# Kernel tuning notes

Measured on AMD Instinct MI355X. Metric: run time of the kernel, lower is better.

Reference implementation:

```python
import jax, jax.numpy as jnp
import numpy as np

B, S = 32, 4096
QRYDIM, CTXDIM, ENCDIM = 512, 512, 256


def setup_inputs() -> dict:
    key = jax.random.key(0)
    ks = jax.random.split(key, 8)
    qry = jax.random.normal(ks[0], (B, QRYDIM), dtype=jnp.float32)
    ctx = jax.random.normal(ks[1], (B, S, CTXDIM), dtype=jnp.float32)
    ctx_mask = jax.random.randint(ks[2], (B, S), 0, 2, dtype=jnp.int32)
    # first Linear(qrydim+ctxdim, encdim): split into ctx-part and qry-part
    # (equivalent to concat([ctx, qry]) @ W1^T since concat order is [ctx, qry])
    sc1 = 1.0 / np.sqrt(QRYDIM + CTXDIM)
    Wc = jax.random.uniform(ks[3], (CTXDIM, ENCDIM), jnp.float32, -sc1, sc1)
    Wq = jax.random.uniform(ks[4], (QRYDIM, ENCDIM), jnp.float32, -sc1, sc1)
    b1 = jax.random.uniform(ks[5], (ENCDIM,), jnp.float32, -sc1, sc1)
    sc2 = 1.0 / np.sqrt(ENCDIM)
    w2 = jax.random.uniform(ks[6], (ENCDIM,), jnp.float32, -sc2, sc2)
    b2 = jax.random.uniform(ks[7], (), jnp.float32, -sc2, sc2)
    return {"qry": qry, "ctx": ctx, "ctx_mask": ctx_mask,
            "Wc": Wc, "Wq": Wq, "b1": b1, "w2": w2, "b2": b2}


def reference(qry, ctx, ctx_mask, Wc, Wq, b1, w2, b2):
    # hidden = tanh(concat([ctx, qry_broadcast]) @ W1 + b1), computed without
    # materializing the (B, S, CTXDIM+QRYDIM) concat tensor
    h_ctx = jnp.einsum('bsc,ce->bse', ctx, Wc)          # (B, S, E)
    h_qry = jnp.einsum('bq,qe->be', qry, Wq)            # (B, E)
    h = jnp.tanh(h_ctx + h_qry[:, None, :] + b1)        # (B, S, E)
    scores = jnp.einsum('bse,e->bs', h, w2) + b2        # (B, S)
    # additive log-mask, then softmax over seqlen
    scores = scores + jnp.log(ctx_mask.astype(jnp.float32))
    alphas = jax.nn.softmax(scores, axis=-1)            # (B, S)
    # weighted sum over context (values default to ctx)
    summary = jnp.einsum('bs,bsd->bd', alphas, ctx)     # (B, CTXDIM)
    return alphas, summary, scores
```

## Files before the change

### kernel.cpp

```cpp
#include <hip/hip_runtime.h>
#include <math.h>

#define BB 32
#define SS 4096
#define CD 512
#define ED 256

#define ALPHAS_OFF 0
#define SUMMARY_OFF (BB * SS)
#define SCORES_OFF (BB * SS + BB * CD)

#define NEG_BIG (-1.0e30f)

typedef __attribute__((ext_vector_type(8))) short short8;
typedef __attribute__((ext_vector_type(8))) unsigned short us8;
typedef __attribute__((ext_vector_type(4))) float f32x4;

__device__ __forceinline__ unsigned short f2bf(float f) {
    unsigned u = __float_as_uint(f);
    u += 0x7FFFu + ((u >> 16) & 1u);
    return (unsigned short)(u >> 16);
}
__device__ __forceinline__ float bf2f(unsigned short h) {
    return __uint_as_float(((unsigned)h) << 16);
}
__device__ __forceinline__ float fast_tanh(float x) {
    const float ex = __expf(2.0f * x);
    return 1.0f - __fdividef(2.0f, ex + 1.0f);
}

#define GLOAD_LDS16(g, l) __builtin_amdgcn_global_load_lds( \
    (const __attribute__((address_space(1))) void*)(g),     \
    (__attribute__((address_space(3))) void*)(l), 16, 0, 0)

#define WS_BH_OFF 32768
#define BPLANE 131072

__global__ void k_prep(const float* __restrict__ Wc, unsigned short* __restrict__ Bh,
                       unsigned short* __restrict__ Bl) {
    const int bid = blockIdx.x;
    const int l = threadIdx.x;
    const int e = (bid & 15) * 16 + (l & 15);
    const int kbase = (bid >> 4) * 32 + (l >> 4) * 8;
    const size_t off = ((size_t)bid * 64 + l) * 8;
#pragma unroll
    for (int j = 0; j < 8; ++j) {
        const float f = Wc[(size_t)(kbase + j) * ED + e];
        const unsigned short h = f2bf(f);
        Bh[off + j] = h;
        Bl[off + j] = f2bf(f - bf2f(h));
    }
}

__global__ void k_hq(const float* __restrict__ qry, const float* __restrict__ Wq,
                     const float* __restrict__ b1, float* __restrict__ hq,
                     float* __restrict__ out) {
    const int b = blockIdx.x;
    const int e = threadIdx.x;
    {
        float* scz = out + SCORES_OFF + b * SS;
#pragma unroll
        for (int i = 0; i < 16; ++i) scz[i * 256 + e] = 0.0f;
    }
    __shared__ float qs[CD];
    qs[e] = qry[b * CD + e];
    qs[e + 256] = qry[b * CD + e + 256];
    __syncthreads();
    float acc = b1[e];
#pragma unroll 8
    for (int c = 0; c < CD; ++c) {
        acc = fmaf(qs[c], Wq[c * ED + e], acc);
    }
    hq[b * ED + e] = acc;
}

#define ST 128
__global__ __launch_bounds__(512, 4)
void k_scores(const float* __restrict__ ctx,
              const unsigned short* __restrict__ Bh, const unsigned short* __restrict__ Bl,
              const float* __restrict__ hq, const float* __restrict__ w2,
              float* __restrict__ out) {
    const int b = blockIdx.y;
    const int stile = blockIdx.x >> 1;
    const int ehalf = blockIdx.x & 1;
    const int s0 = stile * ST;
    const int tid = threadIdx.x;
    const int w = tid >> 6;
    const int l = tid & 63;
    const int eq = w & 1;
    const int mq = w >> 1;

    __shared__ unsigned short BsH[2][8 * 64 * 8];
    __shared__ unsigned short BsL[2][8 * 64 * 8];
    __shared__ float red[2][ST];

    f32x4 acc[2][4];
#pragma unroll
    for (int mi = 0; mi < 2; ++mi)
#pragma unroll
        for (int t = 0; t < 4; ++t) acc[mi][t] = (f32x4)(0.0f);

    const float* ctx_b = ctx + (size_t)(b * SS + s0) * CD;

    const float* aptr0 = ctx_b + (size_t)(mq * 32 + (l & 15)) * CD + (l >> 4) * 8;
    const float* aptr1 = aptr0 + 16 * CD;

    const char* gBplane = (const char*)((w < 4) ? Bh : Bl);
    char* lBbase = (char*)((w < 4) ? &BsH[0][0] : &BsL[0][0]);
    const int wv = w & 3;
    const int bq = wv * 2048 + l * 16;
    const size_t gchunk0 = (size_t)(ehalf * 8) * 1024;

    float4 ra0[2], ra1[2];
    {
        const char* gsrc = gBplane + gchunk0 + bq;
        GLOAD_LDS16(gsrc, lBbase + bq);
        GLOAD_LDS16(gsrc + 1024, lBbase + bq + 1024);
    }
    __builtin_amdgcn_sched_barrier(0);
    ra0[0] = *(const float4*)(aptr0);
    ra1[0] = *(const float4*)(aptr0 + 4);
    ra0[1] = *(const float4*)(aptr1);
    ra1[1] = *(const float4*)(aptr1 + 4);
    __builtin_amdgcn_sched_barrier(0);
    asm volatile("s_waitcnt vmcnt(4)" ::: "memory");
    __builtin_amdgcn_sched_barrier(0);
    __builtin_amdgcn_s_barrier();
    __builtin_amdgcn_sched_barrier(0);

    int cur = 0;
    for (int c = 0; c < 16; ++c) {
        short8 ah[2], alo[2];
#pragma unroll
        for (int mi = 0; mi < 2; ++mi) {
            const float f[8] = {ra0[mi].x, ra0[mi].y, ra0[mi].z, ra0[mi].w,
                                ra1[mi].x, ra1[mi].y, ra1[mi].z, ra1[mi].w};
            short8 H, L;
#pragma unroll
            for (int j = 0; j < 8; ++j) {
                const unsigned short h = f2bf(f[j]);
                H[j] = (short)h;
                L[j] = (short)f2bf(f[j] - bf2f(h));
            }
            ah[mi] = H;
            alo[mi] = L;
        }
        __builtin_amdgcn_sched_barrier(0);

        if (c < 15) {
            const char* gsrc = gBplane + (size_t)(c + 1) * 16384 + gchunk0 + bq;
            char* ldst = lBbase + (cur ^ 1) * 8192 + bq;
            GLOAD_LDS16(gsrc, ldst);
            GLOAD_LDS16(gsrc + 1024, ldst + 1024);
        }
        __builtin_amdgcn_sched_barrier(0);
        if (c < 15) {
            ra0[0] = *(const float4*)(aptr0 + (c + 1) * 32);
            ra1[0] = *(const float4*)(aptr0 + (c + 1) * 32 + 4);
            ra0[1] = *(const float4*)(aptr1 + (c + 1) * 32);
            ra1[1] = *(const float4*)(aptr1 + (c + 1) * 32 + 4);
        }
        __builtin_amdgcn_sched_barrier(0);

        __builtin_amdgcn_s_setprio(1);
#pragma unroll
        for (int t = 0; t < 4; ++t) {
            const int le = eq * 4 + t;
            const int boff = (le * 64 + l) * 8;
            const short8 bh = *(const short8*)(&BsH[cur][boff]);
            const short8 bl = *(const short8*)(&BsL[cur][boff]);
#pragma unroll
            for (int mi = 0; mi < 2; ++mi) {
                acc[mi][t] = __builtin_amdgcn_mfma_f32_16x16x32_bf16(ah[mi], bh, acc[mi][t], 0, 0, 0);
                acc[mi][t] = __builtin_amdgcn_mfma_f32_16x16x32_bf16(alo[mi], bh, acc[mi][t], 0, 0, 0);
                acc[mi][t] = __builtin_amdgcn_mfma_f32_16x16x32_bf16(ah[mi], bl, acc[mi][t], 0, 0, 0);
            }
        }
        __builtin_amdgcn_s_setprio(0);

        __builtin_amdgcn_sched_barrier(0);
        asm volatile("s_waitcnt vmcnt(4)" ::: "memory");
        __builtin_amdgcn_sched_barrier(0);
        __builtin_amdgcn_s_barrier();
        __builtin_amdgcn_sched_barrier(0);
        cur ^= 1;
    }

    float hqr[4], w2r[4];
#pragma unroll
    for (int t = 0; t < 4; ++t) {
        const int e = (ehalf * 8 + eq * 4 + t) * 16 + (l & 15);
        hqr[t] = hq[b * ED + e];
        w2r[t] = w2[e];
    }

#pragma unroll
    for (int mi = 0; mi < 2; ++mi) {
#pragma unroll
        for (int reg = 0; reg < 4; ++reg) {
            float v = 0.0f;
#pragma unroll
            for (int t = 0; t < 4; ++t) {
                v += w2r[t] * fast_tanh(acc[mi][t][reg] + hqr[t]);
            }
            v += __shfl_xor(v, 1, 64);
            v += __shfl_xor(v, 2, 64);
            v += __shfl_xor(v, 4, 64);
            v += __shfl_xor(v, 8, 64);
            if ((l & 15) == 0) {
                const int row = (l >> 4) * 4 + reg;
                red[eq][(mq * 2 + mi) * 16 + row] = v;
            }
        }
    }
    __syncthreads();
    if (tid < ST) {
        atomicAdd(out + SCORES_OFF + b * SS + s0 + tid, red[0][tid] + red[1][tid]);
    }
}

__global__ void k_softmax(float* __restrict__ out, const int* __restrict__ mask,
                          const float* __restrict__ b2p) {
    const int b = blockIdx.x;
    const int tid = threadIdx.x;
    float* sc = out + SCORES_OFF + b * SS;
    float* al = out + ALPHAS_OFF + b * SS;

    {
        float* sm = out + SUMMARY_OFF + b * CD;
        sm[tid] = 0.0f;
        sm[tid + 256] = 0.0f;
    }

    const float b2v = b2p[0];

    __shared__ float red[4];
    __shared__ float bcast;
    const int lane = tid & 63;
    const int wave = tid >> 6;

    float loc[16];
    float mx = -INFINITY;
#pragma unroll
    for (int i = 0; i < 16; ++i) {
        const int s = i * 256 + tid;
        float v = sc[s] + b2v;
        if (mask[b * SS + s] == 0) v = NEG_BIG;
        sc[s] = v;
        loc[i] = v;
        mx = fmaxf(mx, v);
    }
    for (int off = 32; off >= 1; off >>= 1) mx = fmaxf(mx, __shfl_down(mx, off, 64));
    if (lane == 0) red[wave] = mx;
    __syncthreads();
    if (tid == 0) bcast = fmaxf(fmaxf(red[0], red[1]), fmaxf(red[2], red[3]));
    __syncthreads();
    const float mxall = bcast;

    float sum = 0.0f;
#pragma unroll
    for (int i = 0; i < 16; ++i) {
        const float ev = __expf(loc[i] - mxall);
        loc[i] = ev;
        sum += ev;
    }
    for (int off = 32; off >= 1; off >>= 1) sum += __shfl_down(sum, off, 64);
    if (lane == 0) red[wave] = sum;
    __syncthreads();
    if (tid == 0) bcast = red[0] + red[1] + red[2] + red[3];
    __syncthreads();
    const float inv = 1.0f / bcast;

#pragma unroll
    for (int i = 0; i < 16; ++i) al[i * 256 + tid] = loc[i] * inv;
}

#define SROWS 128
__global__ void k_summary(const float* __restrict__ ctx, const float* __restrict__ out_alphas,
                          float* __restrict__ out) {
    const int b = blockIdx.y;
    const int s0 = blockIdx.x * SROWS;
    const int t = threadIdx.x;
    const int sg = t >> 7;
    const int d = (t & 127) * 4;

    __shared__ float al[SROWS];
    if (t < SROWS) al[t] = out_alphas[ALPHAS_OFF + b * SS + s0 + t];
    __syncthreads();

    const float* base = ctx + (size_t)(b * SS + s0 + sg * 64) * CD + d;
    const float* alp = &al[sg * 64];
    float4 a0 = make_float4(0.f, 0.f, 0.f, 0.f);
    float4 a1 = a0, a2 = a0, a3 = a0;
#pragma unroll 2
    for (int i = 0; i < 16; ++i) {
        const int s = i * 4;
        const float w0 = alp[s + 0], w1 = alp[s + 1], w2_ = alp[s + 2], w3 = alp[s + 3];
        if (w0 != 0.0f) {
            const float4 v0 = *(const float4*)(base + (size_t)(s + 0) * CD);
            a0.x = fmaf(w0, v0.x, a0.x); a0.y = fmaf(w0, v0.y, a0.y);
            a0.z = fmaf(w0, v0.z, a0.z); a0.w = fmaf(w0, v0.w, a0.w);
        }
        if (w1 != 0.0f) {
            const float4 v1 = *(const float4*)(base + (size_t)(s + 1) * CD);
            a1.x = fmaf(w1, v1.x, a1.x); a1.y = fmaf(w1, v1.y, a1.y);
            a1.z = fmaf(w1, v1.z, a1.z); a1.w = fmaf(w1, v1.w, a1.w);
        }
        if (w2_ != 0.0f) {
            const float4 v2 = *(const float4*)(base + (size_t)(s + 2) * CD);
            a2.x = fmaf(w2_, v2.x, a2.x); a2.y = fmaf(w2_, v2.y, a2.y);
            a2.z = fmaf(w2_, v2.z, a2.z); a2.w = fmaf(w2_, v2.w, a2.w);
        }
        if (w3 != 0.0f) {
            const float4 v3 = *(const float4*)(base + (size_t)(s + 3) * CD);
            a3.x = fmaf(w3, v3.x, a3.x); a3.y = fmaf(w3, v3.y, a3.y);
            a3.z = fmaf(w3, v3.z, a3.z); a3.w = fmaf(w3, v3.w, a3.w);
        }
    }
    const float rx = (a0.x + a1.x) + (a2.x + a3.x);
    const float ry = (a0.y + a1.y) + (a2.y + a3.y);
    const float rz = (a0.z + a1.z) + (a2.z + a3.z);
    const float rw = (a0.w + a1.w) + (a2.w + a3.w);
    float* dst = out + SUMMARY_OFF + b * CD + d;
    atomicAdd(dst + 0, rx);
    atomicAdd(dst + 1, ry);
    atomicAdd(dst + 2, rz);
    atomicAdd(dst + 3, rw);
}

extern "C" void kernel_launch(void* const* d_in, const int* in_sizes, int n_in,
                              void* d_out, int out_size, void* d_ws, size_t ws_size,
                              hipStream_t stream) {
    const float* qry  = (const float*)d_in[0];
    const float* ctx  = (const float*)d_in[1];
    const int*   msk  = (const int*)d_in[2];
    const float* Wc   = (const float*)d_in[3];
    const float* Wq   = (const float*)d_in[4];
    const float* b1   = (const float*)d_in[5];
    const float* w2   = (const float*)d_in[6];
    const float* b2   = (const float*)d_in[7];
    float* out = (float*)d_out;
    float* hq = (float*)d_ws;
    unsigned short* Bh = (unsigned short*)((char*)d_ws + WS_BH_OFF);
    unsigned short* Bl = Bh + BPLANE;

    k_prep<<<256, 64, 0, stream>>>(Wc, Bh, Bl);
    k_hq<<<BB, ED, 0, stream>>>(qry, Wq, b1, hq, out);
    k_scores<<<dim3(64, BB), 512, 0, stream>>>(ctx, Bh, Bl, hq, w2, out);
    k_softmax<<<BB, 256, 0, stream>>>(out, msk, b2);
    k_summary<<<dim3(SS / SROWS, BB), 256, 0, stream>>>(ctx, out, out);
}
```

Before: 510.2 us.

## Compute full encoder width per score block and use packed bf16 conversion

Each k_scores block now covers all 256 encoder columns instead of half, so each ctx tile is read from global memory and split into bf16 hi/lo parts once rather than twice. Because one block now owns the whole row, scores are written directly, which drops the atomicAdd and the zero-initialisation in k_hq. The fp32-to-bf16 split also uses the packed v_cvt_pk_bf16_f32 instruction in place of manual rounding. In exchange the grid is half as large, and each block uses twice the LDS and accumulator registers, which may lower occupancy under the launch bounds.

```diff
diff --git a/kernel.cpp b/kernel.cpp
--- a/kernel.cpp
+++ b/kernel.cpp
@@ -15,6 +15,7 @@
 typedef __attribute__((ext_vector_type(8))) short short8;
 typedef __attribute__((ext_vector_type(8))) unsigned short us8;
 typedef __attribute__((ext_vector_type(4))) float f32x4;
+typedef union { short8 s8; unsigned u[4]; } fragu;
 
 __device__ __forceinline__ unsigned short f2bf(float f) {
     unsigned u = __float_as_uint(f);
@@ -23,6 +24,11 @@
 }
 __device__ __forceinline__ float bf2f(unsigned short h) {
     return __uint_as_float(((unsigned)h) << 16);
+}
+__device__ __forceinline__ unsigned cvtpk_bf16(float a, float b) {
+    unsigned r;
+    asm("v_cvt_pk_bf16_f32 %0, %1, %2" : "=v"(r) : "v"(a), "v"(b));
+    return r;
 }
 __device__ __forceinline__ float fast_tanh(float x) {
     const float ex = __expf(2.0f * x);
@@ -53,15 +59,9 @@
 }
 
 __global__ void k_hq(const float* __restrict__ qry, const float* __restrict__ Wq,
-                     const float* __restrict__ b1, float* __restrict__ hq,
-                     float* __restrict__ out) {
+                     const float* __restrict__ b1, float* __restrict__ hq) {
     const int b = blockIdx.x;
     const int e = threadIdx.x;
-    {
-        float* scz = out + SCORES_OFF + b * SS;
-#pragma unroll
-        for (int i = 0; i < 16; ++i) scz[i * 256 + e] = 0.0f;
-    }
     __shared__ float qs[CD];
     qs[e] = qry[b * CD + e];
     qs[e + 256] = qry[b * CD + e + 256];
@@ -81,24 +81,22 @@
               const float* __restrict__ hq, const float* __restrict__ w2,
               float* __restrict__ out) {
     const int b = blockIdx.y;
-    const int stile = blockIdx.x >> 1;
-    const int ehalf = blockIdx.x & 1;
-    const int s0 = stile * ST;
+    const int s0 = blockIdx.x * ST;
     const int tid = threadIdx.x;
     const int w = tid >> 6;
     const int l = tid & 63;
     const int eq = w & 1;
     const int mq = w >> 1;
 
-    __shared__ unsigned short BsH[2][8 * 64 * 8];
-    __shared__ unsigned short BsL[2][8 * 64 * 8];
+    __shared__ unsigned short BsH[2][16 * 64 * 8];
+    __shared__ unsigned short BsL[2][16 * 64 * 8];
     __shared__ float red[2][ST];
 
-    f32x4 acc[2][4];
+    f32x4 acc[2][8];
 #pragma unroll
     for (int mi = 0; mi < 2; ++mi)
 #pragma unroll
-        for (int t = 0; t < 4; ++t) acc[mi][t] = (f32x4)(0.0f);
+        for (int t = 0; t < 8; ++t) acc[mi][t] = (f32x4)(0.0f);
 
     const float* ctx_b = ctx + (size_t)(b * SS + s0) * CD;
 
@@ -107,15 +105,15 @@
 
     const char* gBplane = (const char*)((w < 4) ? Bh : Bl);
     char* lBbase = (char*)((w < 4) ? &BsH[0][0] : &BsL[0][0]);
-    const int wv = w & 3;
-    const int bq = wv * 2048 + l * 16;
-    const size_t gchunk0 = (size_t)(ehalf * 8) * 1024;
+    const int bq = (w & 3) * 4096 + l * 16;
 
     float4 ra0[2], ra1[2];
     {
-        const char* gsrc = gBplane + gchunk0 + bq;
+        const char* gsrc = gBplane + bq;
         GLOAD_LDS16(gsrc, lBbase + bq);
         GLOAD_LDS16(gsrc + 1024, lBbase + bq + 1024);
+        GLOAD_LDS16(gsrc + 2048, lBbase + bq + 2048);
+        GLOAD_LDS16(gsrc + 3072, lBbase + bq + 3072);
     }
     __builtin_amdgcn_sched_barrier(0);
     ra0[0] = *(const float4*)(aptr0);
@@ -133,25 +131,30 @@
         short8 ah[2], alo[2];
 #pragma unroll
         for (int mi = 0; mi < 2; ++mi) {
-            const float f[8] = {ra0[mi].x, ra0[mi].y, ra0[mi].z, ra0[mi].w,
-                                ra1[mi].x, ra1[mi].y, ra1[mi].z, ra1[mi].w};
-            short8 H, L;
-#pragma unroll
-            for (int j = 0; j < 8; ++j) {
-                const unsigned short h = f2bf(f[j]);
-                H[j] = (short)h;
-                L[j] = (short)f2bf(f[j] - bf2f(h));
+            const float fa[8] = {ra0[mi].x, ra0[mi].y, ra0[mi].z, ra0[mi].w,
+                                 ra1[mi].x, ra1[mi].y, ra1[mi].z, ra1[mi].w};
+            fragu fh, fl;
+#pragma unroll
+            for (int p = 0; p < 4; ++p) {
+                const float a = fa[2 * p], bb = fa[2 * p + 1];
+                const unsigned hp = cvtpk_bf16(a, bb);
+                fh.u[p] = hp;
+                const float ahf = __uint_as_float(hp << 16);
+                const float bhf = __uint_as_float(hp & 0xffff0000u);
+                fl.u[p] = cvtpk_bf16(a - ahf, bb - bhf);
             }
-            ah[mi] = H;
-            alo[mi] = L;
+            ah[mi] = fh.s8;
+            alo[mi] = fl.s8;
         }
         __builtin_amdgcn_sched_barrier(0);
 
         if (c < 15) {
-            const char* gsrc = gBplane + (size_t)(c + 1) * 16384 + gchunk0 + bq;
-            char* ldst = lBbase + (cur ^ 1) * 8192 + bq;
+            const char* gsrc = gBplane + (size_t)(c + 1) * 16384 + bq;
+            char* ldst = lBbase + (cur ^ 1) * 16384 + bq;
             GLOAD_LDS16(gsrc, ldst);
             GLOAD_LDS16(gsrc + 1024, ldst + 1024);
+            GLOAD_LDS16(gsrc + 2048, ldst + 2048);
+            GLOAD_LDS16(gsrc + 3072, ldst + 3072);
         }
         __builtin_amdgcn_sched_barrier(0);
         if (c < 15) {
@@ -164,9 +167,9 @@
 
         __builtin_amdgcn_s_setprio(1);
 #pragma unroll
-        for (int t = 0; t < 4; ++t) {
-            const int le = eq * 4 + t;
-            const int boff = (le * 64 + l) * 8;
+        for (int t = 0; t < 8; ++t) {
+            const int etile = eq * 8 + t;
+            const int boff = (etile * 64 + l) * 8;
             const short8 bh = *(const short8*)(&BsH[cur][boff]);
             const short8 bl = *(const short8*)(&BsL[cur][boff]);
 #pragma unroll
@@ -186,10 +189,10 @@
         cur ^= 1;
     }
 
-    float hqr[4], w2r[4];
-#pragma unroll
-    for (int t = 0; t < 4; ++t) {
-        const int e = (ehalf * 8 + eq * 4 + t) * 16 + (l & 15);
+    float hqr[8], w2r[8];
+#pragma unroll
+    for (int t = 0; t < 8; ++t) {
+        const int e = (eq * 8 + t) * 16 + (l & 15);
         hqr[t] = hq[b * ED + e];
         w2r[t] = w2[e];
     }
@@ -200,7 +203,7 @@
         for (int reg = 0; reg < 4; ++reg) {
             float v = 0.0f;
 #pragma unroll
-            for (int t = 0; t < 4; ++t) {
+            for (int t = 0; t < 8; ++t) {
                 v += w2r[t] * fast_tanh(acc[mi][t][reg] + hqr[t]);
             }
             v += __shfl_xor(v, 1, 64);
@@ -215,7 +218,7 @@
     }
     __syncthreads();
     if (tid < ST) {
-        atomicAdd(out + SCORES_OFF + b * SS + s0 + tid, red[0][tid] + red[1][tid]);
+        out[SCORES_OFF + b * SS + s0 + tid] = red[0][tid] + red[1][tid];
     }
 }
 
@@ -345,8 +348,8 @@
     unsigned short* Bl = Bh + BPLANE;
 
     k_prep<<<256, 64, 0, stream>>>(Wc, Bh, Bl);
-    k_hq<<<BB, ED, 0, stream>>>(qry, Wq, b1, hq, out);
-    k_scores<<<dim3(64, BB), 512, 0, stream>>>(ctx, Bh, Bl, hq, w2, out);
+    k_hq<<<BB, ED, 0, stream>>>(qry, Wq, b1, hq);
+    k_scores<<<dim3(SS / ST, BB), 512, 0, stream>>>(ctx, Bh, Bl, hq, w2, out);
     k_softmax<<<BB, 256, 0, stream>>>(out, msk, b2);
     k_summary<<<dim3(SS / SROWS, BB), 256, 0, stream>>>(ctx, out, out);
 }
```

Result: faster. 467.0 us (-8.5%).
